# Performance work log

Hardware: AMD Instinct MI355X
Metric: run time of the kernel (lower is better)

The kernel has to match this reference:

```python
import jax, jax.numpy as jnp
import numpy as np

B = 262144
IN, H = 2, 50


def setup_inputs() -> dict:
    key = jax.random.key(0)
    ks = jax.random.split(key, 12)
    k = 1.0 / np.sqrt(H)
    u = lambda kk, shape: jax.random.uniform(kk, shape, jnp.float32, -k, k)
    return {
        "s": jax.random.normal(ks[0], (B, IN), jnp.float32),
        "h": jax.random.normal(ks[1], (B, H), jnp.float32),
        "w_ih": u(ks[2], (3 * H, IN)),
        "w_hh": u(ks[3], (3 * H, H)),
        "b_ih": u(ks[4], (3 * H,)),
        "b_hh": u(ks[5], (3 * H,)),
        "actor_w": u(ks[6], (2, H)),
        "actor_b": u(ks[7], (2,)),
        "critic_w": u(ks[8], (1, H)),
        "critic_b": u(ks[9], (1,)),
    }


def reference(s, h, w_ih, w_hh, b_ih, b_hh, actor_w, actor_b, critic_w, critic_b):
    # PyTorch GRUCell gate math (gate order: reset, update, new)
    gi = s @ w_ih.T + b_ih          # [B, 3H]
    gh = h @ w_hh.T + b_hh          # [B, 3H]
    i_r, i_z, i_n = jnp.split(gi, 3, axis=1)
    h_r, h_z, h_n = jnp.split(gh, 3, axis=1)
    r = jax.nn.sigmoid(i_r + h_r)
    z = jax.nn.sigmoid(i_z + h_z)
    n = jnp.tanh(i_n + r * h_n)
    h_new = (1.0 - z) * n + z * h   # [B, H]
    c = h_new @ critic_w.T + critic_b            # [B, 1]
    pi = jax.nn.softmax(h_new @ actor_w.T + actor_b, axis=1)  # [B, 2]
    return h_new, c, pi
```

## Files before the change

### kernel.cpp

```cpp
#include <hip/hip_runtime.h>
#include <hip/hip_bf16.h>


#define BDIM 1024

typedef __bf16 bf16x8 __attribute__((ext_vector_type(8)));
typedef float f32x4 __attribute__((ext_vector_type(4)));
typedef unsigned __attribute__((may_alias)) u32a;
typedef unsigned short __attribute__((may_alias)) u16a;

__device__ __forceinline__ float bf2f(unsigned short u) {
    union { unsigned u; float f; } x; x.u = ((unsigned)u) << 16; return x.f;
}
__device__ __forceinline__ unsigned short f2bf(float f) {
    union { float f; unsigned u; } x; x.f = f;
    unsigned r = x.u + 0x7fffu + ((x.u >> 16) & 1u);
    return (unsigned short)(r >> 16);
}
__device__ __forceinline__ unsigned packbf(float a, float b) {
    union { __hip_bfloat162 h; unsigned u; } c;
    c.h = __float22bfloat162_rn(make_float2(a, b));
    return c.u;
}
__device__ __forceinline__ bf16x8 ldsfrag(const unsigned short* p) {
    bf16x8 v; __builtin_memcpy(&v, p, 16); return v;
}

template <int CTRL>
__device__ __forceinline__ float dpp_add(float v) {
    int s = __builtin_bit_cast(int, v);
    int r = __builtin_amdgcn_update_dpp(s, s, CTRL, 0xf, 0xf, false);
    return v + __builtin_bit_cast(float, r);
}
__device__ __forceinline__ float row16_sum(float v) {
    v = dpp_add<0x128>(v);
    v = dpp_add<0x124>(v);
    v = dpp_add<0x122>(v);
    v = dpp_add<0x121>(v);
    return v;
}

__global__ __launch_bounds__(BDIM, 4) void gru_fused(
    const float* __restrict__ s,
    const float* __restrict__ h,
    const float* __restrict__ w_ih,
    const float* __restrict__ w_hh,
    const float* __restrict__ b_ih,
    const float* __restrict__ b_hh,
    const float* __restrict__ actor_w,
    const float* __restrict__ actor_b,
    const float* __restrict__ critic_w,
    const float* __restrict__ critic_b,
    float* __restrict__ out,
    int Btot, int nTiles)
{
    __shared__ __align__(16) unsigned short xlds[256 * 72];
    __shared__ __align__(16) unsigned short wlds[1536 * 8];

    const int tid  = threadIdx.x;
    const int wave = tid >> 6;
    const int lane = tid & 63;
    const int c16  = lane & 15;
    const int quad = lane >> 4;
    const int R    = wave * 16;

    u32a* xlds32 = (u32a*)xlds;

    for (int i = tid; i < 256 * 36; i += BDIM)
        xlds32[i] = ((i % 36) == 26) ? 0x00003f80u : 0u;

    for (int e = tid; e < 1536; e += BDIM) {
        int ln = e & 63;
        int ks = (e >> 6) & 1;
        int t  = (e >> 7) & 3;
        int g  = e >> 9;
        int n  = t * 16 + (ln & 15);
        int kbase = ks * 32 + (ln >> 4) * 8;
        unsigned short vals[8];
        if (n < 50) {
            int r = g * 50 + n;
            #pragma unroll
            for (int i = 0; i < 8; ++i) {
                int k = kbase + i;
                float v = 0.f;
                if (k < 50)       v = w_hh[r * 50 + k];
                else if (k == 50) v = (g < 2) ? w_ih[r * 2 + 0] : 0.f;
                else if (k == 51) v = (g < 2) ? w_ih[r * 2 + 1] : 0.f;
                else if (k == 52) {
                    v = b_hh[r];
                    if (g < 2) v += b_ih[r];
                }
                vals[i] = f2bf(v);
            }
        } else {
            #pragma unroll
            for (int i = 0; i < 8; ++i) vals[i] = 0;
        }
        #pragma unroll
        for (int i = 0; i < 8; ++i) wlds[e * 8 + i] = vals[i];
    }

    float wi0[4], wi1[4], bi[4], aw0[4], aw1[4], awc[4];
    #pragma unroll
    for (int t = 0; t < 4; ++t) {
        int j = t * 16 + c16;
        bool ok = (j < 50);
        wi0[t] = ok ? w_ih[(100 + j) * 2 + 0] : 0.f;
        wi1[t] = ok ? w_ih[(100 + j) * 2 + 1] : 0.f;
        bi[t]  = ok ? b_ih[100 + j]           : 0.f;
        aw0[t] = ok ? actor_w[j]              : 0.f;
        aw1[t] = ok ? actor_w[50 + j]         : 0.f;
        awc[t] = ok ? critic_w[j]             : 0.f;
    }
    const float ab0 = actor_b[0], ab1 = actor_b[1], cb = critic_b[0];

    __syncthreads();

    const float2* h2 = (const float2*)h;
    const float2* s2 = (const float2*)s;
    const long long outc = (long long)Btot * 50;
    float2* opi = (float2*)(out + (long long)Btot * 51);

    float2 pf[7];
    int bt = blockIdx.x;
    {
        long long hb = (long long)(bt * 256 + R) * 25;
        #pragma unroll
        for (int j = 0; j < 6; ++j) pf[j] = h2[hb + lane + j * 64];
        if (lane < 16)      pf[6] = h2[hb + 384 + lane];
        else if (lane < 32) pf[6] = s2[bt * 256 + R + lane - 16];
    }

    while (bt < nTiles) {
        const int rowbase = bt * 256;

        #pragma unroll
        for (int j = 0; j < 6; ++j) {
            int d = lane + j * 64;
            int r = d / 25, dk = d - r * 25;
            xlds32[(R + r) * 36 + dk] = packbf(pf[j].x, pf[j].y);
        }
        if (lane < 16)
            xlds32[(R + 15) * 36 + 9 + lane] = packbf(pf[6].x, pf[6].y);
        else if (lane < 32)
            xlds32[(R + lane - 16) * 36 + 25] = packbf(pf[6].x, pf[6].y);

        asm volatile("" ::: "memory");

        const int nbt = bt + gridDim.x;
        {
            int pb = (nbt < nTiles) ? nbt : bt;
            long long hb = (long long)(pb * 256 + R) * 25;
            #pragma unroll
            for (int j = 0; j < 6; ++j) pf[j] = h2[hb + lane + j * 64];
            if (lane < 16)      pf[6] = h2[hb + 384 + lane];
            else if (lane < 32) pf[6] = s2[pb * 256 + R + lane - 16];
        }

        float2 srow[4];
        #pragma unroll
        for (int reg = 0; reg < 4; ++reg)
            srow[reg] = s2[rowbase + R + quad * 4 + reg];

        const unsigned short* arow = &xlds[(R + c16) * 72 + quad * 8];
        bf16x8 a0 = ldsfrag(arow);
        bf16x8 a1 = ldsfrag(arow + 32);

        float hn_r[4][4];
        #pragma unroll
        for (int t = 0; t < 4; ++t) {
            f32x4 ar = {0.f,0.f,0.f,0.f}, az = ar, an = ar;
            const int tb = (t * 128 + lane) * 8;
            bf16x8 br0 = ldsfrag(&wlds[tb]);
            bf16x8 br1 = ldsfrag(&wlds[tb + 512]);
            bf16x8 bz0 = ldsfrag(&wlds[tb + 4096]);
            bf16x8 bz1 = ldsfrag(&wlds[tb + 4608]);
            bf16x8 bn0 = ldsfrag(&wlds[tb + 8192]);
            bf16x8 bn1 = ldsfrag(&wlds[tb + 8704]);
            ar = __builtin_amdgcn_mfma_f32_16x16x32_bf16(a0, br0, ar, 0, 0, 0);
            ar = __builtin_amdgcn_mfma_f32_16x16x32_bf16(a1, br1, ar, 0, 0, 0);
            az = __builtin_amdgcn_mfma_f32_16x16x32_bf16(a0, bz0, az, 0, 0, 0);
            az = __builtin_amdgcn_mfma_f32_16x16x32_bf16(a1, bz1, az, 0, 0, 0);
            an = __builtin_amdgcn_mfma_f32_16x16x32_bf16(a0, bn0, an, 0, 0, 0);
            an = __builtin_amdgcn_mfma_f32_16x16x32_bf16(a1, bn1, an, 0, 0, 0);

            int j = t * 16 + c16;
            #pragma unroll
            for (int reg = 0; reg < 4; ++reg) {
                int lr = R + quad * 4 + reg;
                float inn = fmaf(srow[reg].y, wi1[t],
                            fmaf(srow[reg].x, wi0[t], bi[t]));
                float rg = __builtin_amdgcn_rcpf(1.f + __expf(-ar[reg]));
                float zg = __builtin_amdgcn_rcpf(1.f + __expf(-az[reg]));
                float x = inn + rg * an[reg];
                x = fminf(fmaxf(x, -20.f), 20.f);
                float e2 = __expf(2.f * x);
                float ng = (e2 - 1.f) * __builtin_amdgcn_rcpf(e2 + 1.f);
                float hv = bf2f(((const u16a*)xlds)[lr * 72 + j]);
                float hnew = (1.f - zg) * ng + zg * hv;
                bool ok = (j < 50);
                hn_r[reg][t] = ok ? hnew : 0.f;
                if (ok) out[(long long)(rowbase + lr) * 50 + j] = hnew;
            }
        }

        float sum0[4], sum1[4], sumc[4];
        #pragma unroll
        for (int reg = 0; reg < 4; ++reg) {
            float p0 = 0.f, p1 = 0.f, pc = 0.f;
            #pragma unroll
            for (int t = 0; t < 4; ++t) {
                p0 = fmaf(hn_r[reg][t], aw0[t], p0);
                p1 = fmaf(hn_r[reg][t], aw1[t], p1);
                pc = fmaf(hn_r[reg][t], awc[t], pc);
            }
            sum0[reg] = row16_sum(p0);
            sum1[reg] = row16_sum(p1);
            sumc[reg] = row16_sum(pc);
        }
        if (c16 < 4) {
            float A0 = (c16 == 0) ? sum0[0] : (c16 == 1) ? sum0[1]
                     : (c16 == 2) ? sum0[2] : sum0[3];
            float A1 = (c16 == 0) ? sum1[0] : (c16 == 1) ? sum1[1]
                     : (c16 == 2) ? sum1[2] : sum1[3];
            float C  = (c16 == 0) ? sumc[0] : (c16 == 1) ? sumc[1]
                     : (c16 == 2) ? sumc[2] : sumc[3];
            int gr = rowbase + R + quad * 4 + c16;
            out[outc + gr] = C + cb;
            A0 += ab0; A1 += ab1;
            float m = fmaxf(A0, A1);
            float e0 = __expf(A0 - m), e1 = __expf(A1 - m);
            float inv = 1.f / (e0 + e1);
            float2 pv; pv.x = e0 * inv; pv.y = e1 * inv;
            opi[gr] = pv;
        }
        bt = nbt;
    }
}

extern "C" void kernel_launch(void* const* d_in, const int* in_sizes, int n_in,
                              void* d_out, int out_size, void* d_ws, size_t ws_size,
                              hipStream_t stream) {
    const float* s        = (const float*)d_in[0];
    const float* h        = (const float*)d_in[1];
    const float* w_ih     = (const float*)d_in[2];
    const float* w_hh     = (const float*)d_in[3];
    const float* b_ih     = (const float*)d_in[4];
    const float* b_hh     = (const float*)d_in[5];
    const float* actor_w  = (const float*)d_in[6];
    const float* actor_b  = (const float*)d_in[7];
    const float* critic_w = (const float*)d_in[8];
    const float* critic_b = (const float*)d_in[9];
    float* out = (float*)d_out;

    int Btot = in_sizes[1] / 50;
    int nTiles = Btot / 256;
    int grid = nTiles < 512 ? nTiles : 512;

    gru_fused<<<grid, BDIM, 0, stream>>>(s, h, w_ih, w_hh, b_ih, b_hh,
                                         actor_w, actor_b, critic_w, critic_b,
                                         out, Btot, nTiles);
}
```

Measured before the change: 142.4 us.

## Issue both tiles' global loads before weight staging, fixed two tiles per block

Replaces the grid-stride persistent loop with a fixed two-tile-per-block schedule. Both tiles' h/s loads are issued at kernel entry, before the LDS init and weight staging, so the global-memory latency overlaps the setup work. The grid becomes nTiles/2 (512 for this size), so the block count is unchanged but the loop and prefetch bookkeeping go away. It also drops the tanh clamp and folds the h_new blend into a single fma. Without the clamp, very large inputs could give inf/NaN in the tanh path, and holding two prefetch buffers raises register pressure.

```diff
diff --git a/kernel.cpp b/kernel.cpp
--- a/kernel.cpp
+++ b/kernel.cpp
@@ -39,6 +39,95 @@
     v = dpp_add<0x121>(v);
     return v;
 }
+
+#define PROCESS_TILE(BT, PF)                                                 \
+  do {                                                                       \
+    const int rowbase = (BT) * 256;                                          \
+    asm volatile("" ::: "memory");                                           \
+    _Pragma("unroll")                                                        \
+    for (int j = 0; j < 6; ++j) {                                            \
+        int d = lane + j * 64;                                               \
+        int r = d / 25, dk = d - r * 25;                                     \
+        xlds32[(R + r) * 36 + dk] = packbf(PF[j].x, PF[j].y);                \
+    }                                                                        \
+    if (lane < 16)                                                           \
+        xlds32[(R + 15) * 36 + 9 + lane] = packbf(PF[6].x, PF[6].y);         \
+    else if (lane < 32)                                                      \
+        xlds32[(R + lane - 16) * 36 + 25] = packbf(PF[6].x, PF[6].y);        \
+    asm volatile("" ::: "memory");                                           \
+    float2 srow[4];                                                          \
+    _Pragma("unroll")                                                        \
+    for (int reg = 0; reg < 4; ++reg)                                        \
+        srow[reg] = s2[rowbase + R + quad * 4 + reg];                        \
+    const unsigned short* arow = &xlds[(R + c16) * 72 + quad * 8];           \
+    bf16x8 a0 = ldsfrag(arow);                                 \
+    bf16x8 a1 = ldsfrag(arow + 32);                            \
+    float* ob = out + (long long)rowbase * 50;      \
+    float hn_r[4][4];                                                        \
+    _Pragma("unroll")                                                        \
+    for (int t = 0; t < 4; ++t) {                                            \
+        f32x4 ar = {0.f,0.f,0.f,0.f}, az = ar, an = ar;                      \
+        const int tb = (t * 128 + lane) * 8;   \
+        bf16x8 br0 = ldsfrag(&wlds[tb]);                                     \
+        bf16x8 br1 = ldsfrag(&wlds[tb + 512]);                               \
+        bf16x8 bz0 = ldsfrag(&wlds[tb + 4096]);                              \
+        bf16x8 bz1 = ldsfrag(&wlds[tb + 4608]);                              \
+        bf16x8 bn0 = ldsfrag(&wlds[tb + 8192]);                              \
+        bf16x8 bn1 = ldsfrag(&wlds[tb + 8704]);                              \
+        ar = __builtin_amdgcn_mfma_f32_16x16x32_bf16(a0, br0, ar, 0, 0, 0);  \
+        ar = __builtin_amdgcn_mfma_f32_16x16x32_bf16(a1, br1, ar, 0, 0, 0);  \
+        az = __builtin_amdgcn_mfma_f32_16x16x32_bf16(a0, bz0, az, 0, 0, 0);  \
+        az = __builtin_amdgcn_mfma_f32_16x16x32_bf16(a1, bz1, az, 0, 0, 0);  \
+        an = __builtin_amdgcn_mfma_f32_16x16x32_bf16(a0, bn0, an, 0, 0, 0);  \
+        an = __builtin_amdgcn_mfma_f32_16x16x32_bf16(a1, bn1, an, 0, 0, 0);  \
+        int j = t * 16 + c16;                                                \
+        _Pragma("unroll")                                                    \
+        for (int reg = 0; reg < 4; ++reg) {                                  \
+            int lr = R + quad * 4 + reg;          \
+            float inn = fmaf(srow[reg].y, wi1[t],                            \
+                        fmaf(srow[reg].x, wi0[t], bi[t]));                   \
+            float rg = __builtin_amdgcn_rcpf(1.f + __expf(-ar[reg]));        \
+            float zg = __builtin_amdgcn_rcpf(1.f + __expf(-az[reg]));        \
+            float x = inn + rg * an[reg];                                    \
+            float e2 = __expf(2.f * x);    \
+            float ng = 1.f - 2.f * __builtin_amdgcn_rcpf(e2 + 1.f);          \
+            float hv = bf2f(((const u16a*)xlds)[lr * 72 + j]);               \
+            float hnew = fmaf(zg, hv - ng, ng);                              \
+            hn_r[reg][t] = (j < 50) ? hnew : 0.f;                            \
+            if (j < 50) ob[lr * 50 + j] = hnew;                              \
+        }                                                                    \
+    }                                                                        \
+    float sum0[4], sum1[4], sumc[4];                                         \
+    _Pragma("unroll")                                                        \
+    for (int reg = 0; reg < 4; ++reg) {                                      \
+        float p0 = 0.f, p1 = 0.f, pc = 0.f;                                  \
+        _Pragma("unroll")                                                    \
+        for (int t = 0; t < 4; ++t) {                                        \
+            p0 = fmaf(hn_r[reg][t], aw0[t], p0);                             \
+            p1 = fmaf(hn_r[reg][t], aw1[t], p1);                             \
+            pc = fmaf(hn_r[reg][t], awc[t], pc);                             \
+        }                                                                    \
+        sum0[reg] = row16_sum(p0);                                           \
+        sum1[reg] = row16_sum(p1);                                           \
+        sumc[reg] = row16_sum(pc);                                           \
+    }                                                                        \
+    if (c16 < 4) {                  \
+        float A0 = (c16 == 0) ? sum0[0] : (c16 == 1) ? sum0[1]               \
+                 : (c16 == 2) ? sum0[2] : sum0[3];                           \
+        float A1 = (c16 == 0) ? sum1[0] : (c16 == 1) ? sum1[1]               \
+                 : (c16 == 2) ? sum1[2] : sum1[3];                           \
+        float C  = (c16 == 0) ? sumc[0] : (c16 == 1) ? sumc[1]               \
+                 : (c16 == 2) ? sumc[2] : sumc[3];                           \
+        int gr = rowbase + R + quad * 4 + c16;                               \
+        oc[gr] = C + cb;                                                     \
+        A0 += ab0; A1 += ab1;                                                \
+        float m = fmaxf(A0, A1);                                             \
+        float e0 = __expf(A0 - m), e1 = __expf(A1 - m);                      \
+        float inv = 1.f / (e0 + e1);                                         \
+        float2 pv; pv.x = e0 * inv; pv.y = e1 * inv;                         \
+        opi[gr] = pv;                                                        \
+    }                                                                        \
+  } while (0)
 
 __global__ __launch_bounds__(BDIM, 4) void gru_fused(
     const float* __restrict__ s,
@@ -65,6 +154,28 @@
     const int R    = wave * 16;
 
     u32a* xlds32 = (u32a*)xlds;
+    const float2* h2 = (const float2*)h;
+    const float2* s2 = (const float2*)s;
+
+    const int bt0 = blockIdx.x;
+    const int bt1 = bt0 + (int)gridDim.x;
+    const bool has2 = (bt1 < nTiles);
+    float2 pf0[7], pf1[7];
+    {
+        long long hb = (long long)(bt0 * 256 + R) * 25;
+        #pragma unroll
+        for (int j = 0; j < 6; ++j) pf0[j] = h2[hb + lane + j * 64];
+        if (lane < 16)      pf0[6] = h2[hb + 384 + lane];
+        else if (lane < 32) pf0[6] = s2[bt0 * 256 + R + lane - 16];
+    }
+    {
+        const int pb = has2 ? bt1 : bt0;
+        long long hb = (long long)(pb * 256 + R) * 25;
+        #pragma unroll
+        for (int j = 0; j < 6; ++j) pf1[j] = h2[hb + lane + j * 64];
+        if (lane < 16)      pf1[6] = h2[hb + 384 + lane];
+        else if (lane < 32) pf1[6] = s2[pb * 256 + R + lane - 16];
+    }
 
     for (int i = tid; i < 256 * 36; i += BDIM)
         xlds32[i] = ((i % 36) == 26) ? 0x00003f80u : 0u;
@@ -116,126 +227,11 @@
 
     __syncthreads();
 
-    const float2* h2 = (const float2*)h;
-    const float2* s2 = (const float2*)s;
-    const long long outc = (long long)Btot * 50;
+    float* oc = out + (long long)Btot * 50;
     float2* opi = (float2*)(out + (long long)Btot * 51);
 
-    float2 pf[7];
-    int bt = blockIdx.x;
-    {
-        long long hb = (long long)(bt * 256 + R) * 25;
-        #pragma unroll
-        for (int j = 0; j < 6; ++j) pf[j] = h2[hb + lane + j * 64];
-        if (lane < 16)      pf[6] = h2[hb + 384 + lane];
-        else if (lane < 32) pf[6] = s2[bt * 256 + R + lane - 16];
-    }
-
-    while (bt < nTiles) {
-        const int rowbase = bt * 256;
-
-        #pragma unroll
-        for (int j = 0; j < 6; ++j) {
-            int d = lane + j * 64;
-            int r = d / 25, dk = d - r * 25;
-            xlds32[(R + r) * 36 + dk] = packbf(pf[j].x, pf[j].y);
-        }
-        if (lane < 16)
-            xlds32[(R + 15) * 36 + 9 + lane] = packbf(pf[6].x, pf[6].y);
-        else if (lane < 32)
-            xlds32[(R + lane - 16) * 36 + 25] = packbf(pf[6].x, pf[6].y);
-
-        asm volatile("" ::: "memory");
-
-        const int nbt = bt + gridDim.x;
-        {
-            int pb = (nbt < nTiles) ? nbt : bt;
-            long long hb = (long long)(pb * 256 + R) * 25;
-            #pragma unroll
-            for (int j = 0; j < 6; ++j) pf[j] = h2[hb + lane + j * 64];
-            if (lane < 16)      pf[6] = h2[hb + 384 + lane];
-            else if (lane < 32) pf[6] = s2[pb * 256 + R + lane - 16];
-        }
-
-        float2 srow[4];
-        #pragma unroll
-        for (int reg = 0; reg < 4; ++reg)
-            srow[reg] = s2[rowbase + R + quad * 4 + reg];
-
-        const unsigned short* arow = &xlds[(R + c16) * 72 + quad * 8];
-        bf16x8 a0 = ldsfrag(arow);
-        bf16x8 a1 = ldsfrag(arow + 32);
-
-        float hn_r[4][4];
-        #pragma unroll
-        for (int t = 0; t < 4; ++t) {
-            f32x4 ar = {0.f,0.f,0.f,0.f}, az = ar, an = ar;
-            const int tb = (t * 128 + lane) * 8;
-            bf16x8 br0 = ldsfrag(&wlds[tb]);
-            bf16x8 br1 = ldsfrag(&wlds[tb + 512]);
-            bf16x8 bz0 = ldsfrag(&wlds[tb + 4096]);
-            bf16x8 bz1 = ldsfrag(&wlds[tb + 4608]);
-            bf16x8 bn0 = ldsfrag(&wlds[tb + 8192]);
-            bf16x8 bn1 = ldsfrag(&wlds[tb + 8704]);
-            ar = __builtin_amdgcn_mfma_f32_16x16x32_bf16(a0, br0, ar, 0, 0, 0);
-            ar = __builtin_amdgcn_mfma_f32_16x16x32_bf16(a1, br1, ar, 0, 0, 0);
-            az = __builtin_amdgcn_mfma_f32_16x16x32_bf16(a0, bz0, az, 0, 0, 0);
-            az = __builtin_amdgcn_mfma_f32_16x16x32_bf16(a1, bz1, az, 0, 0, 0);
-            an = __builtin_amdgcn_mfma_f32_16x16x32_bf16(a0, bn0, an, 0, 0, 0);
-            an = __builtin_amdgcn_mfma_f32_16x16x32_bf16(a1, bn1, an, 0, 0, 0);
-
-            int j = t * 16 + c16;
-            #pragma unroll
-            for (int reg = 0; reg < 4; ++reg) {
-                int lr = R + quad * 4 + reg;
-                float inn = fmaf(srow[reg].y, wi1[t],
-                            fmaf(srow[reg].x, wi0[t], bi[t]));
-                float rg = __builtin_amdgcn_rcpf(1.f + __expf(-ar[reg]));
-                float zg = __builtin_amdgcn_rcpf(1.f + __expf(-az[reg]));
-                float x = inn + rg * an[reg];
-                x = fminf(fmaxf(x, -20.f), 20.f);
-                float e2 = __expf(2.f * x);
-                float ng = (e2 - 1.f) * __builtin_amdgcn_rcpf(e2 + 1.f);
-                float hv = bf2f(((const u16a*)xlds)[lr * 72 + j]);
-                float hnew = (1.f - zg) * ng + zg * hv;
-                bool ok = (j < 50);
-                hn_r[reg][t] = ok ? hnew : 0.f;
-                if (ok) out[(long long)(rowbase + lr) * 50 + j] = hnew;
-            }
-        }
-
-        float sum0[4], sum1[4], sumc[4];
-        #pragma unroll
-        for (int reg = 0; reg < 4; ++reg) {
-            float p0 = 0.f, p1 = 0.f, pc = 0.f;
-            #pragma unroll
-            for (int t = 0; t < 4; ++t) {
-                p0 = fmaf(hn_r[reg][t], aw0[t], p0);
-                p1 = fmaf(hn_r[reg][t], aw1[t], p1);
-                pc = fmaf(hn_r[reg][t], awc[t], pc);
-            }
-            sum0[reg] = row16_sum(p0);
-            sum1[reg] = row16_sum(p1);
-            sumc[reg] = row16_sum(pc);
-        }
-        if (c16 < 4) {
-            float A0 = (c16 == 0) ? sum0[0] : (c16 == 1) ? sum0[1]
-                     : (c16 == 2) ? sum0[2] : sum0[3];
-            float A1 = (c16 == 0) ? sum1[0] : (c16 == 1) ? sum1[1]
-                     : (c16 == 2) ? sum1[2] : sum1[3];
-            float C  = (c16 == 0) ? sumc[0] : (c16 == 1) ? sumc[1]
-                     : (c16 == 2) ? sumc[2] : sumc[3];
-            int gr = rowbase + R + quad * 4 + c16;
-            out[outc + gr] = C + cb;
-            A0 += ab0; A1 += ab1;
-            float m = fmaxf(A0, A1);
-            float e0 = __expf(A0 - m), e1 = __expf(A1 - m);
-            float inv = 1.f / (e0 + e1);
-            float2 pv; pv.x = e0 * inv; pv.y = e1 * inv;
-            opi[gr] = pv;
-        }
-        bt = nbt;
-    }
+    PROCESS_TILE(bt0, pf0);
+    if (has2) PROCESS_TILE(bt1, pf1);
 }
 
 extern "C" void kernel_launch(void* const* d_in, const int* in_sizes, int n_in,
@@ -255,7 +251,7 @@
 
     int Btot = in_sizes[1] / 50;
     int nTiles = Btot / 256;
-    int grid = nTiles < 512 ? nTiles : 512;
+    int grid = (nTiles + 1) / 2;
 
     gru_fused<<<grid, BDIM, 0, stream>>>(s, h, w_ih, w_hh, b_ih, b_hh,
                                          actor_w, actor_b, critic_w, critic_b,
```

Result: no change. 144.6 us (+1.6%).
